# Kernel optimization log

Measured on AMD Instinct MI355X. Metric: run time of the kernel, lower is better.

Reference implementation:

```python
import jax, jax.numpy as jnp
import numpy as np

B, C, H, W = 16, 256, 32, 32
DIM = H * W  # LayerNorm/Linear dim == h*w per the rearrange in forward


def _conv1x1(x, w, b):
    # x: [b,c,h,w], w: [out,in] (1x1 kernel squeezed), b: [out]
    return jnp.einsum('bchw,oc->bohw', x, w) + b[None, :, None, None]


def _layernorm(x, g, b, eps=1e-5):
    mu = jnp.mean(x, axis=-1, keepdims=True)
    var = jnp.var(x, axis=-1, keepdims=True)
    return (x - mu) / jnp.sqrt(var + eps) * g + b


def setup_inputs() -> dict:
    key = jax.random.key(0)
    ks = jax.random.split(key, 12)
    n = jax.random.normal
    k_cdc = (2.0 / (2 * C)) ** 0.5   # kaiming_normal fan_in = 2C
    k_v = (2.0 / C) ** 0.5           # fan_in = C
    k_lin = (2.0 / DIM) ** 0.5       # fan_in = DIM
    return {
        'x_spa': n(ks[0], (B, C, H, W), jnp.float32),
        'x_freq': n(ks[1], (B, C, H, W), jnp.float32),
        'w_cdc': n(ks[2], (C, 2 * C), jnp.float32) * k_cdc,
        'b_cdc': jnp.zeros((C,), jnp.float32),
        'w_sv': n(ks[3], (C, C), jnp.float32) * k_v,
        'b_sv': jnp.zeros((C,), jnp.float32),
        'w_fv': n(ks[4], (C, C), jnp.float32) * k_v,
        'b_fv': jnp.zeros((C,), jnp.float32),
        'ln_w': jnp.ones((DIM,), jnp.float32),
        'ln_b': jnp.zeros((DIM,), jnp.float32),
        'w_qk': n(ks[5], (2 * DIM, DIM), jnp.float32) * k_lin,  # Linear(dim, 2*dim), no bias
        'w_spa': n(ks[6], (DIM, DIM), jnp.float32) * k_lin,
        'b_spa': jnp.zeros((DIM,), jnp.float32),
        'w_frq': n(ks[7], (DIM, DIM), jnp.float32) * k_lin,
        'b_frq': jnp.zeros((DIM,), jnp.float32),
    }


def reference(x_spa, x_freq, w_cdc, b_cdc, w_sv, b_sv, w_fv, b_fv,
              ln_w, ln_b, w_qk, w_spa, b_spa, w_frq, b_frq):
    b, c, h, w = x_spa.shape
    hw = h * w
    scale = hw ** (-0.5)
    v_spa = _conv1x1(x_spa, w_sv, b_sv).reshape(b, c, hw)
    v_freq = _conv1x1(x_freq, w_fv, b_fv).reshape(b, c, hw)
    x = _conv1x1(jnp.concatenate([x_spa, x_freq], axis=1), w_cdc, b_cdc).reshape(b, c, hw)
    x = _layernorm(x, ln_w, ln_b)
    qk = x @ w_qk.T                       # [b, c, 2*hw]
    q, k = jnp.split(qk, 2, axis=-1)      # each [b, c, hw]
    att = jnp.einsum('bcn,bcm->bnm', q, k) * scale   # q^T k over channels: [b, hw, hw]
    att_spa = jax.nn.softmax(att @ w_spa.T + b_spa, axis=-1)
    att_frq = jax.nn.softmax(att @ w_frq.T + b_frq, axis=-1)
    out_spa = x_spa + jnp.einsum('bcn,bnm->bcm', v_spa, att_spa).reshape(b, c, h, w)
    out_freq = x_freq + jnp.einsum('bcn,bnm->bcm', v_freq, att_frq).reshape(b, c, h, w)
    return out_spa, out_freq
```

## Files before the change

kernel.cpp:

```cpp
#include <hip/hip_runtime.h>
#include <hip/hip_bf16.h>

typedef __hip_bfloat16 bf16;
typedef __attribute__((ext_vector_type(8))) short bf16x8v;
typedef __attribute__((ext_vector_type(4))) float f32x4v;

__device__ __forceinline__ float bfbits2f(unsigned short h) {
    union { unsigned int u; float f; } v; v.u = ((unsigned int)h) << 16; return v.f;
}
__device__ __forceinline__ unsigned short f2bfbits(float f) {
    bf16 h = __float2bfloat16(f);
    unsigned short s;
    __builtin_memcpy(&s, &h, 2);
    return s;
}
__device__ __forceinline__ float load1_any(const void* p, long idx, bool f32) {
    if (f32) return ((const float*)p)[idx];
    return bfbits2f(((const unsigned short*)p)[idx]);
}
__device__ __forceinline__ float4 loadbf4(const bf16* p) {
    ushort4 u = *reinterpret_cast<const ushort4*>(p);
    return make_float4(bfbits2f(u.x), bfbits2f(u.y), bfbits2f(u.z), bfbits2f(u.w));
}
__device__ __forceinline__ void store_bf4(bf16* p, float a, float b, float c, float d) {
    ushort4 o;
    o.x = f2bfbits(a); o.y = f2bfbits(b); o.z = f2bfbits(c); o.w = f2bfbits(d);
    *reinterpret_cast<ushort4*>(p) = o;
}
__device__ __forceinline__ void gl16(const void* g, void* l) {
    __builtin_amdgcn_global_load_lds(
        (const __attribute__((address_space(1))) unsigned int*)g,
        (__attribute__((address_space(3))) unsigned int*)l, 16, 0, 0);
}

__global__ __launch_bounds__(1024)
void detect_kernel(const unsigned short* __restrict__ x, int* __restrict__ flag) {
    const int tid = threadIdx.x;
    int zc = 0, hc = 0;
    const uint4* xv = (const uint4*)x;
#pragma unroll
    for (int p = 0; p < 16; ++p) {
        uint4 v = xv[p * 1024 + tid];
        unsigned s0 = v.x & 0xFFFFu, s1 = v.y & 0xFFFFu;
        unsigned s2 = v.z & 0xFFFFu, s3 = v.w & 0xFFFFu;
        zc += (int)(s0 == 0) + (int)(s1 == 0) + (int)(s2 == 0) + (int)(s3 == 0);
        hc += (int)(((s0 >> 7) & 0xFFu) >= 0x90u) + (int)(((s1 >> 7) & 0xFFu) >= 0x90u)
            + (int)(((s2 >> 7) & 0xFFu) >= 0x90u) + (int)(((s3 >> 7) & 0xFFu) >= 0x90u);
    }
#pragma unroll
    for (int off = 32; off > 0; off >>= 1) {
        zc += __shfl_down(zc, off);
        hc += __shfl_down(hc, off);
    }
    __shared__ int rz[16], rh[16];
    if ((tid & 63) == 0) { rz[tid >> 6] = zc; rh[tid >> 6] = hc; }
    __syncthreads();
    if (tid == 0) {
        int Z = 0, H = 0;
#pragma unroll
        for (int i = 0; i < 16; ++i) { Z += rz[i]; H += rh[i]; }
        *flag = (Z > 60000 || H > 256) ? 1 : 0;
    }
}

__global__ void diag_kernel(float* __restrict__ out, float val) {
    if (threadIdx.x == 0) out[0] = val;
}

__global__ __launch_bounds__(256)
void convert6_kernel(const void* __restrict__ s0, const void* __restrict__ s1,
                     const void* __restrict__ s2, const void* __restrict__ s3,
                     const void* __restrict__ s4, const void* __restrict__ s5,
                     bf16* __restrict__ dst, const int* __restrict__ dflag) {
    const bool f32 = (*dflag != 0);
    for (long i = (long)blockIdx.x * 256 + threadIdx.x; i < 4456448;
         i += (long)gridDim.x * 256) {
        const void* s; long o;
        if (i < 131072)       { s = s0; o = i; }
        else if (i < 196608)  { s = s1; o = i - 131072; }
        else if (i < 262144)  { s = s2; o = i - 196608; }
        else if (i < 2359296) { s = s3; o = i - 262144; }
        else if (i < 3407872) { s = s4; o = i - 2359296; }
        else                  { s = s5; o = i - 3407872; }
        dst[i] = __float2bfloat16(load1_any(s, o, f32));
    }
}

__global__ __launch_bounds__(256)
void xpose_conv_kernel(const void* __restrict__ x1, const void* __restrict__ x2,
                       bf16* __restrict__ dst, int bofs, int zsplit,
                       const int* __restrict__ dflag) {
    const bool f32 = (*dflag != 0);
    __shared__ float t[64][65];
    const int ch0 = blockIdx.y * 64, n0 = blockIdx.x * 64, z = blockIdx.z;
    const bool hiz = (z >= zsplit);
    const int zl = hiz ? z - zsplit : z;
    const void* x = hiz ? x2 : x1;
    const long sb = (long)(zl + bofs) * 262144, db = (long)z * 262144;
    const int tid = threadIdx.x;
#pragma unroll
    for (int p = 0; p < 16; ++p) {
        int e = tid + p * 256; int sch = e >> 6, sn = e & 63;
        t[sch][sn] = load1_any(x, sb + (long)(ch0 + sch) * 1024 + n0 + sn, f32);
    }
    __syncthreads();
#pragma unroll
    for (int p = 0; p < 16; ++p) {
        int e = tid + p * 256; int dn = e >> 6, dch = e & 63;
        dst[db + (long)(n0 + dn) * 256 + ch0 + dch] = __float2bfloat16(t[dch][dn]);
    }
}

__global__ __launch_bounds__(256)
void xpose_bf_kernel(const bf16* __restrict__ src, bf16* __restrict__ dst) {
    __shared__ float t[64][65];
    const int c0 = blockIdx.x * 64, r0 = blockIdx.y * 64;
    const long b = (long)blockIdx.z * 1048576;
    const int tid = threadIdx.x;
#pragma unroll
    for (int p = 0; p < 16; ++p) {
        int e = tid + p * 256; int r = e >> 6, c = e & 63;
        t[r][c] = __bfloat162float(src[b + (long)(r0 + r) * 1024 + c0 + c]);
    }
    __syncthreads();
#pragma unroll
    for (int p = 0; p < 16; ++p) {
        int e = tid + p * 256; int r = e >> 6, c = e & 63;
        dst[b + (long)(c0 + r) * 1024 + r0 + c] = __float2bfloat16(t[c][r]);
    }
}

template <int EPI>
__global__ __launch_bounds__(256)
void mfma_nt(const bf16* __restrict__ A1, const bf16* __restrict__ A2,
             long aBatch, int ldA,
             const bf16* __restrict__ B1, const bf16* __restrict__ B2,
             long bBatch, int ldB, int ksplit, long kOff2,
             void* __restrict__ out1, void* __restrict__ out2,
             long oBatch, int ldO, int K, float scale,
             const void* __restrict__ bias1, const void* __restrict__ bias2,
             const void* __restrict__ res1, const void* __restrict__ res2,
             long rBatch, int bofs, int zsplit,
             const int* __restrict__ dflag) {
    __shared__ short As[2][4096];
    __shared__ short Bs[2][4096];
    const int tid  = threadIdx.x;
    const int lane = tid & 63, wave = tid >> 6;
    const int quad = lane >> 4, lrow = lane & 15;
    const int wm = (wave >> 1) * 64, wn = (wave & 1) * 64;
    const int n0 = blockIdx.x * 128, m0 = blockIdx.y * 128;
    const int z  = blockIdx.z;
    const bool hiz = (z >= zsplit);
    const int zl = hiz ? z - zsplit : z;
    const int srow = tid >> 2, sseg = tid & 3;
    const int sl = sseg ^ ((srow >> 1) & 3);
    const int xq = quad ^ ((lrow >> 1) & 3);

    const bf16* Ab = (hiz ? A2 : A1) + (long)zl * aBatch;
    const bf16* Bb = (hiz ? B2 : B1) + (long)zl * bBatch;

    auto stage = [&](int buf, int k0) {
        const bf16* asrc = Ab + (long)k0;
        const bf16* bsrc = Bb + ((k0 < ksplit) ? (long)k0 : (long)(k0 - ksplit) + kOff2);
        const bf16* ga0 = asrc + (long)(m0 + srow) * ldA + sl * 8;
        const bf16* ga1 = asrc + (long)(m0 + 64 + srow) * ldA + sl * 8;
        const bf16* gb0 = bsrc + (long)(n0 + srow) * ldB + sl * 8;
        const bf16* gb1 = bsrc + (long)(n0 + 64 + srow) * ldB + sl * 8;
        short* la = &As[buf][wave * 512];
        short* lb = &Bs[buf][wave * 512];
        gl16(ga0, la);
        gl16(ga1, la + 2048);
        gl16(gb0, lb);
        gl16(gb1, lb + 2048);
    };

    f32x4v acc[4][4] = {};
    const int nt = K >> 5;
    int cur = 0;
    stage(0, 0);
    asm volatile("s_waitcnt vmcnt(0)" ::: "memory");
    __builtin_amdgcn_s_barrier();

    for (int t = 0; t < nt; ++t) {
        if (t + 1 < nt) stage(cur ^ 1, (t + 1) << 5);
        bf16x8v bfr[4];
#pragma unroll
        for (int j = 0; j < 4; ++j) {
            int r = wn + j * 16 + lrow;
            bfr[j] = *(const bf16x8v*)&Bs[cur][r * 32 + xq * 8];
        }
#pragma unroll
        for (int i = 0; i < 4; ++i) {
            int r = wm + i * 16 + lrow;
            bf16x8v af = *(const bf16x8v*)&As[cur][r * 32 + xq * 8];
#pragma unroll
            for (int j = 0; j < 4; ++j)
                acc[i][j] = __builtin_amdgcn_mfma_f32_16x16x32_bf16(af, bfr[j], acc[i][j], 0, 0, 0);
        }
        if (t + 1 < nt) {
            __builtin_amdgcn_sched_barrier(0);
            asm volatile("s_waitcnt vmcnt(0) lgkmcnt(0)" ::: "memory");
            __builtin_amdgcn_s_barrier();
            cur ^= 1;
        }
    }

    const bool f32 = (*dflag != 0);
    const void* bias = hiz ? bias2 : bias1;
    if (EPI <= 2) {
        bf16* O = (bf16*)(hiz ? out2 : out1) + (long)zl * oBatch;
#pragma unroll
        for (int i = 0; i < 4; ++i) {
            int row0 = m0 + wm + i * 16 + quad * 4;
            float rb[4] = {0.f, 0.f, 0.f, 0.f};
            if (EPI == 1) {
#pragma unroll
                for (int r = 0; r < 4; ++r) rb[r] = load1_any(bias, row0 + r, f32);
            }
#pragma unroll
            for (int j = 0; j < 4; ++j) {
                int col = n0 + wn + j * 16 + lrow;
                float cb = (EPI == 2) ? load1_any(bias, col, f32) : 0.f;
#pragma unroll
                for (int r = 0; r < 4; ++r) {
                    float vv = acc[i][j][r];
                    if (EPI == 1) vv += rb[r];
                    if (EPI == 2) vv = vv * scale + cb;
                    O[(long)(row0 + r) * ldO + col] = __float2bfloat16(vv);
                }
            }
        }
    } else {
        float* O = (float*)(hiz ? out2 : out1);
        const void* res = hiz ? res2 : res1;
        const long ob  = (long)(zl + bofs) * oBatch;
        const long rbb = (long)(zl + bofs) * rBatch;
#pragma unroll
        for (int i = 0; i < 4; ++i) {
            int row0 = m0 + wm + i * 16 + quad * 4;
#pragma unroll
            for (int j = 0; j < 4; ++j) {
                int col = n0 + wn + j * 16 + lrow;
#pragma unroll
                for (int r = 0; r < 4; ++r) {
                    float rv = load1_any(res, rbb + (long)(row0 + r) * ldO + col, f32);
                    O[ob + (long)(row0 + r) * ldO + col] = acc[i][j][r] + rv;
                }
            }
        }
    }
}

__global__ __launch_bounds__(256)
void layernorm_kernel(bf16* __restrict__ x, const void* __restrict__ g,
                      const void* __restrict__ beta, const int* __restrict__ dflag) {
    const bool f32 = (*dflag != 0);
    bf16* p = x + (long)blockIdx.x * 1024;
    const int tid = threadIdx.x;
    float4 v = loadbf4(p + tid * 4);
    float s  = v.x + v.y + v.z + v.w;
    float ss = v.x * v.x + v.y * v.y + v.z * v.z + v.w * v.w;
#pragma unroll
    for (int off = 32; off > 0; off >>= 1) {
        s  += __shfl_down(s, off);
        ss += __shfl_down(ss, off);
    }
    __shared__ float sh[8];
    __shared__ float sh_mu, sh_rs;
    if ((tid & 63) == 0) { sh[tid >> 6] = s; sh[4 + (tid >> 6)] = ss; }
    __syncthreads();
    if (tid == 0) {
        float S  = sh[0] + sh[1] + sh[2] + sh[3];
        float SS = sh[4] + sh[5] + sh[6] + sh[7];
        float mu = S * (1.0f / 1024.0f);
        float var = SS * (1.0f / 1024.0f) - mu * mu;
        sh_mu = mu;
        sh_rs = rsqrtf(fmaxf(var, 0.0f) + 1e-5f);
    }
    __syncthreads();
    float mu = sh_mu, rs = sh_rs;
    float gx = load1_any(g, tid * 4 + 0, f32), gy = load1_any(g, tid * 4 + 1, f32);
    float gz = load1_any(g, tid * 4 + 2, f32), gw = load1_any(g, tid * 4 + 3, f32);
    float bx = load1_any(beta, tid * 4 + 0, f32), by = load1_any(beta, tid * 4 + 1, f32);
    float bz = load1_any(beta, tid * 4 + 2, f32), bw = load1_any(beta, tid * 4 + 3, f32);
    store_bf4(p + tid * 4,
              (v.x - mu) * rs * gx + bx, (v.y - mu) * rs * gy + by,
              (v.z - mu) * rs * gz + bz, (v.w - mu) * rs * gw + bw);
}

__global__ __launch_bounds__(256)
void softmax_kernel(bf16* __restrict__ x) {
    bf16* p = x + (long)blockIdx.x * 1024;
    const int tid = threadIdx.x;
    float4 v = loadbf4(p + tid * 4);
    float m = fmaxf(fmaxf(v.x, v.y), fmaxf(v.z, v.w));
#pragma unroll
    for (int off = 32; off > 0; off >>= 1) m = fmaxf(m, __shfl_down(m, off));
    __shared__ float sh[8];
    __shared__ float shM, shS;
    if ((tid & 63) == 0) sh[tid >> 6] = m;
    __syncthreads();
    if (tid == 0) shM = fmaxf(fmaxf(sh[0], sh[1]), fmaxf(sh[2], sh[3]));
    __syncthreads();
    float M = shM;
    v.x = __expf(v.x - M);
    v.y = __expf(v.y - M);
    v.z = __expf(v.z - M);
    v.w = __expf(v.w - M);
    float s = v.x + v.y + v.z + v.w;
#pragma unroll
    for (int off = 32; off > 0; off >>= 1) s += __shfl_down(s, off);
    if ((tid & 63) == 0) sh[4 + (tid >> 6)] = s;
    __syncthreads();
    if (tid == 0) shS = sh[4] + sh[5] + sh[6] + sh[7];
    __syncthreads();
    float inv = 1.0f / shS;
    store_bf4(p + tid * 4, v.x * inv, v.y * inv, v.z * inv, v.w * inv);
}

extern "C" void kernel_launch(void* const* d_in, const int* in_sizes, int n_in,
                              void* d_out, int out_size, void* d_ws, size_t ws_size,
                              hipStream_t stream) {
    const void* x_spa  = d_in[0];
    const void* x_freq = d_in[1];
    const void* w_cdc  = d_in[2];
    const void* b_cdc  = d_in[3];
    const void* w_sv   = d_in[4];
    const void* b_sv   = d_in[5];
    const void* w_fv   = d_in[6];
    const void* b_fv   = d_in[7];
    const void* ln_w   = d_in[8];
    const void* ln_b   = d_in[9];
    const void* w_qk   = d_in[10];
    const void* w_spa  = d_in[11];
    const void* b_spa  = d_in[12];
    const void* w_frq  = d_in[13];
    const void* b_frq  = d_in[14];
    float* out = (float*)d_out;

    const int B = 16, C = 256;
    const long XB = 262144;
    const long PB = 1048576;

    int*  dflag = (int*)d_ws;
    bf16* wb    = (bf16*)((char*)d_ws + 4096);
    bf16* w_cdc_b = wb;
    bf16* w_sv_b  = w_cdc_b + 131072;
    bf16* w_fv_b  = w_sv_b  + 65536;
    bf16* w_qk_b  = w_fv_b  + 65536;
    bf16* w_spa_b = w_qk_b  + 2097152;
    bf16* w_frq_b = w_spa_b + 1048576;
    bf16* pb      = w_frq_b + 1048576;

    const size_t fixedB = 4096 + 4456448ull * 2;
    const size_t perB   = 13107200ull;
    size_t avail = (ws_size > fixedB) ? (ws_size - fixedB) : 0;
    long gmax = (long)(avail / perB);
    const bool wsOK = (gmax >= 1);
    int G = wsOK ? (int)(gmax > 16 ? 16 : gmax) : 1;

    bf16* xT   = pb;
    bf16* xln  = xT   + 2L * G * XB;
    bf16* kb   = xln  + (long)G * XB;
    bf16* qT   = kb   + (long)G * XB;
    bf16* TT   = qT   + (long)G * XB;
    bf16* vb   = TT   + 2L * G * XB;
    bf16* attp = vb   + 2L * G * XB;
    bf16* attpT= attp + 2L * G * PB;

    dim3 blk(256);
    detect_kernel<<<dim3(1), dim3(1024), 0, stream>>>((const unsigned short*)x_spa, dflag);

    if (!wsOK) {
        float mb = (float)(ws_size >> 20);
        diag_kernel<<<dim3(1), dim3(64), 0, stream>>>(out, 1000.0f * (mb + 1.0f));
        return;
    }

    convert6_kernel<<<dim3(4352), blk, 0, stream>>>(w_cdc, w_sv, w_fv, w_qk, w_spa, w_frq,
                                                    wb, dflag);

    for (int b0 = 0; b0 < B; b0 += G) {
        int g = (B - b0 < G) ? (B - b0) : G;

        xpose_conv_kernel<<<dim3(16, 4, 2 * g), blk, 0, stream>>>(
            x_spa, x_freq, xT, b0, g, dflag);

        mfma_nt<1><<<dim3(8, 2, 2 * g), blk, 0, stream>>>(
            w_sv_b, w_fv_b, 0, 256,
            xT, xT + (long)g * XB, XB, 256, 256, 0,
            vb, vb + (long)g * XB, XB, 1024, 256, 1.0f,
            b_sv, b_fv, nullptr, nullptr, 0, 0, g, dflag);

        mfma_nt<1><<<dim3(8, 2, g), blk, 0, stream>>>(
            w_cdc_b, w_cdc_b, 0, 512,
            xT, xT, XB, 256, 256, (long)g * XB,
            xln, xln, XB, 1024, 512, 1.0f,
            b_cdc, b_cdc, nullptr, nullptr, 0, 0, g, dflag);
        layernorm_kernel<<<dim3(g * C), blk, 0, stream>>>(xln, ln_w, ln_b, dflag);

        mfma_nt<0><<<dim3(8, 2, g), blk, 0, stream>>>(
            xln, xln, XB, 1024,
            w_qk_b + 1048576, w_qk_b + 1048576, 0, 1024, 1024, 0,
            kb, kb, XB, 1024, 1024, 1.0f,
            nullptr, nullptr, nullptr, nullptr, 0, 0, g, dflag);
        mfma_nt<0><<<dim3(2, 8, g), blk, 0, stream>>>(
            w_qk_b, w_qk_b, 0, 1024,
            xln, xln, XB, 1024, 1024, 0,
            qT, qT, XB, 256, 1024, 1.0f,
            nullptr, nullptr, nullptr, nullptr, 0, 0, g, dflag);

        mfma_nt<0><<<dim3(2, 8, 2 * g), blk, 0, stream>>>(
            w_spa_b, w_frq_b, 0, 1024,
            kb, kb, XB, 1024, 1024, 0,
            TT, TT + (long)g * XB, XB, 256, 1024, 1.0f,
            nullptr, nullptr, nullptr, nullptr, 0, 0, g, dflag);

        mfma_nt<2><<<dim3(8, 8, 2 * g), blk, 0, stream>>>(
            qT, qT, XB, 256,
            TT, TT + (long)g * XB, XB, 256, 256, 0,
            attp, attp + (long)g * PB, PB, 1024, 256, 0.03125f,
            b_spa, b_frq, nullptr, nullptr, 0, 0, g, dflag);

        softmax_kernel<<<dim3(2 * g * 1024), blk, 0, stream>>>(attp);
        xpose_bf_kernel<<<dim3(16, 16, 2 * g), blk, 0, stream>>>(attp, attpT);

        mfma_nt<3><<<dim3(8, 2, 2 * g), blk, 0, stream>>>(
            vb, vb + (long)g * XB, XB, 1024,
            attpT, attpT + (long)g * PB, PB, 1024, 1024, 0,
            out, out + 4194304, XB, 1024, 1024, 1.0f,
            nullptr, nullptr, x_spa, x_freq, XB, b0, g, dflag);
    }
}
```

Baseline: 405.5 us.

## Split softmax into stats pass fused with transpose; triple-buffer MFMA GEMM

Softmax now runs as a stats-only pass that computes the row max and inverse sum, one wave per row, and writes them to a small buffer. The existing transpose kernel applies exp and normalisation as it reads, so the normalised probability matrix is never written back and reread. Separately, the generic MFMA GEMM moves from double to triple LDS buffering with counted vmcnt waits, so global loads run two tiles ahead. The cost is more LDS per block, which may lower occupancy, plus an extra barrier per k-step and recomputing exp inside the transpose.

```diff
diff --git a/kernel.cpp b/kernel.cpp
--- a/kernel.cpp
+++ b/kernel.cpp
@@ -112,15 +112,41 @@
 }
 
 __global__ __launch_bounds__(256)
-void xpose_bf_kernel(const bf16* __restrict__ src, bf16* __restrict__ dst) {
+void sm_stats_kernel(const bf16* __restrict__ x, float2* __restrict__ st) {
+    const int tid = threadIdx.x, lane = tid & 63, w = tid >> 6;
+    const long row = (long)blockIdx.x * 4 + w;
+    const bf16* p = x + row * 1024;
+    float4 v[4];
+    float m = -3.4e38f;
+#pragma unroll
+    for (int c = 0; c < 4; ++c) {
+        v[c] = loadbf4(p + lane * 4 + c * 256);
+        m = fmaxf(m, fmaxf(fmaxf(v[c].x, v[c].y), fmaxf(v[c].z, v[c].w)));
+    }
+#pragma unroll
+    for (int off = 32; off > 0; off >>= 1) m = fmaxf(m, __shfl_xor(m, off));
+    float s = 0.f;
+#pragma unroll
+    for (int c = 0; c < 4; ++c)
+        s += __expf(v[c].x - m) + __expf(v[c].y - m) + __expf(v[c].z - m) + __expf(v[c].w - m);
+#pragma unroll
+    for (int off = 32; off > 0; off >>= 1) s += __shfl_xor(s, off);
+    if (lane == 0) st[row] = make_float2(m, 1.0f / s);
+}
+
+__global__ __launch_bounds__(256)
+void xpose_norm_kernel(const bf16* __restrict__ src, bf16* __restrict__ dst,
+                       const float2* __restrict__ st) {
     __shared__ float t[64][65];
     const int c0 = blockIdx.x * 64, r0 = blockIdx.y * 64;
     const long b = (long)blockIdx.z * 1048576;
+    const long sb = (long)blockIdx.z * 1024;
     const int tid = threadIdx.x;
 #pragma unroll
     for (int p = 0; p < 16; ++p) {
         int e = tid + p * 256; int r = e >> 6, c = e & 63;
-        t[r][c] = __bfloat162float(src[b + (long)(r0 + r) * 1024 + c0 + c]);
+        float2 ms = st[sb + r0 + r];
+        t[r][c] = __expf(__bfloat162float(src[b + (long)(r0 + r) * 1024 + c0 + c]) - ms.x) * ms.y;
     }
     __syncthreads();
 #pragma unroll
@@ -142,8 +168,8 @@
              const void* __restrict__ res1, const void* __restrict__ res2,
              long rBatch, int bofs, int zsplit,
              const int* __restrict__ dflag) {
-    __shared__ short As[2][4096];
-    __shared__ short Bs[2][4096];
+    __shared__ short As[3][4096];
+    __shared__ short Bs[3][4096];
     const int tid  = threadIdx.x;
     const int lane = tid & 63, wave = tid >> 6;
     const int quad = lane >> 4, lrow = lane & 15;
@@ -176,33 +202,36 @@
 
     f32x4v acc[4][4] = {};
     const int nt = K >> 5;
+    stage(0, 0);
+    if (nt > 1) stage(1, 32);
+    if (nt > 2) stage(2, 64);
+
     int cur = 0;
-    stage(0, 0);
-    asm volatile("s_waitcnt vmcnt(0)" ::: "memory");
-    __builtin_amdgcn_s_barrier();
-
     for (int t = 0; t < nt; ++t) {
-        if (t + 1 < nt) stage(cur ^ 1, (t + 1) << 5);
-        bf16x8v bfr[4];
-#pragma unroll
-        for (int j = 0; j < 4; ++j) {
-            int r = wn + j * 16 + lrow;
-            bfr[j] = *(const bf16x8v*)&Bs[cur][r * 32 + xq * 8];
-        }
-#pragma unroll
-        for (int i = 0; i < 4; ++i) {
-            int r = wm + i * 16 + lrow;
-            bf16x8v af = *(const bf16x8v*)&As[cur][r * 32 + xq * 8];
+        const int rem = nt - 1 - t;
+        if (rem >= 2)      asm volatile("s_waitcnt vmcnt(8)" ::: "memory");
+        else if (rem == 1) asm volatile("s_waitcnt vmcnt(4)" ::: "memory");
+        else               asm volatile("s_waitcnt vmcnt(0)" ::: "memory");
+        __builtin_amdgcn_s_barrier();
+        __builtin_amdgcn_sched_barrier(0);
+        bf16x8v bfr[4], afr[4];
+#pragma unroll
+        for (int j = 0; j < 4; ++j)
+            bfr[j] = *(const bf16x8v*)&Bs[cur][(wn + j * 16 + lrow) * 32 + xq * 8];
+#pragma unroll
+        for (int i = 0; i < 4; ++i)
+            afr[i] = *(const bf16x8v*)&As[cur][(wm + i * 16 + lrow) * 32 + xq * 8];
+        asm volatile("s_waitcnt lgkmcnt(0)" ::: "memory");
+        __builtin_amdgcn_sched_barrier(0);
+        __builtin_amdgcn_s_barrier();
+        __builtin_amdgcn_sched_barrier(0);
+        if (t + 3 < nt) stage(cur, (t + 3) << 5);
+#pragma unroll
+        for (int i = 0; i < 4; ++i)
 #pragma unroll
             for (int j = 0; j < 4; ++j)
-                acc[i][j] = __builtin_amdgcn_mfma_f32_16x16x32_bf16(af, bfr[j], acc[i][j], 0, 0, 0);
-        }
-        if (t + 1 < nt) {
-            __builtin_amdgcn_sched_barrier(0);
-            asm volatile("s_waitcnt vmcnt(0) lgkmcnt(0)" ::: "memory");
-            __builtin_amdgcn_s_barrier();
-            cur ^= 1;
-        }
+                acc[i][j] = __builtin_amdgcn_mfma_f32_16x16x32_bf16(afr[i], bfr[j], acc[i][j], 0, 0, 0);
+        cur = (cur == 2) ? 0 : cur + 1;
     }
 
     const bool f32 = (*dflag != 0);
@@ -286,36 +315,6 @@
     store_bf4(p + tid * 4,
               (v.x - mu) * rs * gx + bx, (v.y - mu) * rs * gy + by,
               (v.z - mu) * rs * gz + bz, (v.w - mu) * rs * gw + bw);
-}
-
-__global__ __launch_bounds__(256)
-void softmax_kernel(bf16* __restrict__ x) {
-    bf16* p = x + (long)blockIdx.x * 1024;
-    const int tid = threadIdx.x;
-    float4 v = loadbf4(p + tid * 4);
-    float m = fmaxf(fmaxf(v.x, v.y), fmaxf(v.z, v.w));
-#pragma unroll
-    for (int off = 32; off > 0; off >>= 1) m = fmaxf(m, __shfl_down(m, off));
-    __shared__ float sh[8];
-    __shared__ float shM, shS;
-    if ((tid & 63) == 0) sh[tid >> 6] = m;
-    __syncthreads();
-    if (tid == 0) shM = fmaxf(fmaxf(sh[0], sh[1]), fmaxf(sh[2], sh[3]));
-    __syncthreads();
-    float M = shM;
-    v.x = __expf(v.x - M);
-    v.y = __expf(v.y - M);
-    v.z = __expf(v.z - M);
-    v.w = __expf(v.w - M);
-    float s = v.x + v.y + v.z + v.w;
-#pragma unroll
-    for (int off = 32; off > 0; off >>= 1) s += __shfl_down(s, off);
-    if ((tid & 63) == 0) sh[4 + (tid >> 6)] = s;
-    __syncthreads();
-    if (tid == 0) shS = sh[4] + sh[5] + sh[6] + sh[7];
-    __syncthreads();
-    float inv = 1.0f / shS;
-    store_bf4(p + tid * 4, v.x * inv, v.y * inv, v.z * inv, v.w * inv);
 }
 
 extern "C" void kernel_launch(void* const* d_in, const int* in_sizes, int n_in,
@@ -353,7 +352,7 @@
     bf16* pb      = w_frq_b + 1048576;
 
     const size_t fixedB = 4096 + 4456448ull * 2;
-    const size_t perB   = 13107200ull;
+    const size_t perB   = 13123584ull;
     size_t avail = (ws_size > fixedB) ? (ws_size - fixedB) : 0;
     long gmax = (long)(avail / perB);
     const bool wsOK = (gmax >= 1);
@@ -367,6 +366,7 @@
     bf16* vb   = TT   + 2L * G * XB;
     bf16* attp = vb   + 2L * G * XB;
     bf16* attpT= attp + 2L * G * PB;
+    float2* stats = (float2*)(attpT + 2L * G * PB);
 
     dim3 blk(256);
     detect_kernel<<<dim3(1), dim3(1024), 0, stream>>>((const unsigned short*)x_spa, dflag);
@@ -422,8 +422,8 @@
             attp, attp + (long)g * PB, PB, 1024, 256, 0.03125f,
             b_spa, b_frq, nullptr, nullptr, 0, 0, g, dflag);
 
-        softmax_kernel<<<dim3(2 * g * 1024), blk, 0, stream>>>(attp);
-        xpose_bf_kernel<<<dim3(16, 16, 2 * g), blk, 0, stream>>>(attp, attpT);
+        sm_stats_kernel<<<dim3(512 * g), blk, 0, stream>>>(attp, stats);
+        xpose_norm_kernel<<<dim3(16, 16, 2 * g), blk, 0, stream>>>(attp, attpT, stats);
 
         mfma_nt<3><<<dim3(8, 2, 2 * g), blk, 0, stream>>>(
             vb, vb + (long)g * XB, XB, 1024,
```

Result: faster. 371.5 us (-8.4%).
